# Performance work log

Hardware: AMD Instinct MI355X
Metric: run time of the kernel (lower is better)

The kernel has to match this reference:

```python
import jax, jax.numpy as jnp
import numpy as np

DIM = 1024
HEADS = 16
HEAD_DIM = DIM // HEADS  # 64
B, T, S = 4, 2048, 2048
NEG = -1e9


def rotary_pos_emb(x, freqs):
    # x: (B, H, L, Dh), freqs: (L, Dh//2). Rotate interleaved (even, odd) pairs.
    cos = jnp.cos(freqs)[None, None, :, :]  # (1,1,L,Dh//2)
    sin = jnp.sin(freqs)[None, None, :, :]
    x_even = x[..., 0::2]
    x_odd = x[..., 1::2]
    r_even = x_even * cos - x_odd * sin
    r_odd = x_even * sin + x_odd * cos
    return jnp.stack([r_even, r_odd], axis=-1).reshape(x.shape)


def setup_inputs() -> dict:
    key = jax.random.key(0)
    ks = jax.random.split(key, 9)
    w_std = 1.0 / np.sqrt(DIM)
    return {
        "q_x": jax.random.normal(ks[0], (B, T, DIM), jnp.float32),
        "kv_x": jax.random.normal(ks[1], (B, S, DIM), jnp.float32),
        "freq_q": jax.random.normal(ks[2], (T, HEAD_DIM // 2), jnp.float32),
        "freq_kv": jax.random.normal(ks[3], (S, HEAD_DIM // 2), jnp.float32),
        "key_padding_mask": jax.random.randint(ks[4], (B, S), 0, 2, jnp.int32),
        "Wq": jax.random.normal(ks[5], (DIM, DIM), jnp.float32) * w_std,
        "Wk": jax.random.normal(ks[6], (DIM, DIM), jnp.float32) * w_std,
        "Wv": jax.random.normal(ks[7], (DIM, DIM), jnp.float32) * w_std,
        "Wproj": jax.random.normal(ks[8], (DIM, DIM), jnp.float32) * w_std,
    }


def reference(q_x, kv_x, freq_q, freq_kv, key_padding_mask, Wq, Wk, Wv, Wproj):
    b, t, d = q_x.shape
    s = kv_x.shape[1]
    # QKV projections (torch Linear: x @ W.T), split into heads -> (B, H, L, Dh)
    q = (q_x @ Wq.T).reshape(b, t, HEADS, HEAD_DIM).transpose(0, 2, 1, 3)
    k = (kv_x @ Wk.T).reshape(b, s, HEADS, HEAD_DIM).transpose(0, 2, 1, 3)
    v = (kv_x @ Wv.T).reshape(b, s, HEADS, HEAD_DIM).transpose(0, 2, 1, 3)
    # Rotary embedding on q and k
    q = rotary_pos_emb(q, freq_q)
    k = rotary_pos_emb(k, freq_kv)
    # Scaled dot-product attention with key-padding mask (True = attend)
    scale = HEAD_DIM ** (-0.5)
    scores = jnp.einsum('bhtd,bhsd->bhts', q, k) * scale
    mask = key_padding_mask.astype(bool)[:, None, None, :]  # (B,1,1,S)
    scores = jnp.where(mask, scores, NEG)
    attn = jax.nn.softmax(scores, axis=-1)
    out = jnp.einsum('bhts,bhsd->bhtd', attn, v)
    out = out.transpose(0, 2, 1, 3).reshape(b, t, d)
    return out @ Wproj.T
```

## Files before the change

### kernel.cpp

```cpp
#include <hip/hip_runtime.h>
#include <hip/hip_bf16.h>


typedef __bf16 bf16;
typedef __bf16 bf16x8 __attribute__((ext_vector_type(8)));
typedef __bf16 bf16x4 __attribute__((ext_vector_type(4)));
typedef float  f32x4  __attribute__((ext_vector_type(4)));

#define NB   4
#define NT   2048
#define NS   2048
#define NH   16
#define HD   64
#define SCL  0.18033688011112043f

__device__ __forceinline__ void gload16(const void* g, void* l) {
  __builtin_amdgcn_global_load_lds((const __attribute__((address_space(1))) void*)g,
                                   (__attribute__((address_space(3))) void*)l, 16, 0, 0);
}

__device__ __forceinline__ f32x4 mfma16(bf16x8 a, bf16x8 b, f32x4 c) {
  return __builtin_amdgcn_mfma_f32_16x16x32_bf16(a, b, c, 0, 0, 0);
}

__global__ void k_convert(const float* __restrict__ qx, const float* __restrict__ kvx,
                          const float* __restrict__ Wq, const float* __restrict__ Wk,
                          const float* __restrict__ Wv, const float* __restrict__ Wp,
                          bf16* __restrict__ wbf, bf16* __restrict__ qxbf,
                          bf16* __restrict__ kvxbf)
{
  const long total = 4194304L + 8388608L + 8388608L;
  for (long v = (long)blockIdx.x * blockDim.x + threadIdx.x; v * 4 < total;
       v += (long)gridDim.x * blockDim.x) {
    long e0 = v * 4;
    const float* src; bf16* dst;
    if (e0 < 4194304L) {
      int widx = (int)(e0 >> 20);
      const float* wsrc = (widx == 0) ? Wq : (widx == 1) ? Wk : (widx == 2) ? Wv : Wp;
      src = wsrc + (e0 & 1048575); dst = wbf + e0;
    } else if (e0 < 12582912L) {
      src = qx + (e0 - 4194304L); dst = qxbf + (e0 - 4194304L);
    } else {
      src = kvx + (e0 - 12582912L); dst = kvxbf + (e0 - 12582912L);
    }
    float4 f = *(const float4*)src;
    bf16x4 o = {(bf16)f.x, (bf16)f.y, (bf16)f.z, (bf16)f.w};
    *(bf16x4*)dst = o;
  }
}

__global__ void k_tables(const float* __restrict__ fq, const float* __restrict__ fkv,
                         const int* __restrict__ mask,
                         float2* __restrict__ csq, float2* __restrict__ cskv,
                         float* __restrict__ bias)
{
  int i = blockIdx.x * blockDim.x + threadIdx.x;
  if (i < 65536) {
    float s, c; sincosf(fq[i], &s, &c); csq[i] = make_float2(c, s);
  } else if (i < 131072) {
    int j = i - 65536;
    float s, c; sincosf(fkv[j], &s, &c); cskv[j] = make_float2(c, s);
  } else if (i < 139264) {
    int j = i - 131072;
    bias[j] = mask[j] ? 0.0f : -1.0e9f;
  }
}

template<int EPI>
__global__ __launch_bounds__(256) void k_gemm(
    const bf16* __restrict__ A0, const bf16* __restrict__ A1,
    const bf16* __restrict__ wbase,
    bf16* __restrict__ Qb, bf16* __restrict__ Kb, bf16* __restrict__ Vtb,
    float* __restrict__ Of,
    const float2* __restrict__ csq, const float2* __restrict__ cskv)
{
  __shared__ bf16 As[128 * 32];
  __shared__ bf16 Bs[128 * 32];
  const int z  = (EPI == 0) ? blockIdx.z : 0;
  const bf16* A = (EPI == 1) ? A0 : ((z == 0) ? A0 : A1);
  const bf16* W = wbase + (size_t)z * 1048576;
  const int m0 = blockIdx.x * 128, n0 = blockIdx.y * 128;
  const int tid = threadIdx.x, lane = tid & 63, w = tid >> 6;
  const int g = lane >> 4, c = lane & 15;
  const int wr = w >> 1, wc = w & 1;

  f32x4 acc[4][4];
#pragma unroll
  for (int i = 0; i < 4; ++i)
#pragma unroll
    for (int j = 0; j < 4; ++j) acc[i][j] = 0.0f;

  const bf16* gA = A + (size_t)(m0 + w * 32 + (lane >> 2)) * 1024 + (lane & 3) * 8;
  const bf16* gB = W + (size_t)(n0 + w * 32 + (lane >> 2)) * 1024 + (lane & 3) * 8;
  bf16* lA = As + w * 1024;
  bf16* lB = Bs + w * 1024;

  for (int k0 = 0; k0 < 1024; k0 += 32) {
    __syncthreads();
    gload16(gA, lA);               gload16(gA + 16 * 1024, lA + 512);
    gload16(gB, lB);               gload16(gB + 16 * 1024, lB + 512);
    gA += 32; gB += 32;
    __syncthreads();

    bf16x8 af[4], bfr[4];
#pragma unroll
    for (int mi = 0; mi < 4; ++mi)
      af[mi] = *(const bf16x8*)(As + (wr * 64 + mi * 16 + c) * 32 + g * 8);
#pragma unroll
    for (int ni = 0; ni < 4; ++ni)
      bfr[ni] = *(const bf16x8*)(Bs + (wc * 64 + ni * 16 + c) * 32 + g * 8);
#pragma unroll
    for (int mi = 0; mi < 4; ++mi)
#pragma unroll
      for (int ni = 0; ni < 4; ++ni)
        acc[mi][ni] = mfma16(af[mi], bfr[ni], acc[mi][ni]);
  }

  if (EPI == 1) {
#pragma unroll
    for (int mi = 0; mi < 4; ++mi)
#pragma unroll
      for (int ni = 0; ni < 4; ++ni)
#pragma unroll
        for (int r = 0; r < 4; ++r) {
          int m = m0 + wr * 64 + mi * 16 + g * 4 + r;
          int n = n0 + wc * 64 + ni * 16 + c;
          Of[(size_t)m * 1024 + n] = acc[mi][ni][r];
        }
  } else if (z < 2) {
    const float2* cs = (z == 0) ? csq : cskv;
    bf16* Out = (z == 0) ? Qb : Kb;
#pragma unroll
    for (int mi = 0; mi < 4; ++mi)
#pragma unroll
      for (int ni = 0; ni < 4; ++ni)
#pragma unroll
        for (int r = 0; r < 4; ++r) {
          int m = m0 + wr * 64 + mi * 16 + g * 4 + r;
          int n = n0 + wc * 64 + ni * 16 + c;
          float v = acc[mi][ni][r];
          float p = __shfl_xor(v, 1);
          int t = m & 2047, b = m >> 11;
          int h = n >> 6, d = n & 63;
          float2 cv = cs[t * 32 + (d >> 1)];
          float rot = (d & 1) ? (v * cv.x + p * cv.y)
                              : (v * cv.x - p * cv.y);
          Out[((size_t)((b * 16 + h) * 2048 + t)) * 64 + d] = (bf16)rot;
        }
  } else {
#pragma unroll
    for (int mi = 0; mi < 4; ++mi)
#pragma unroll
      for (int ni = 0; ni < 4; ++ni) {
        int m = m0 + wr * 64 + mi * 16 + g * 4;
        int n = n0 + wc * 64 + ni * 16 + c;
        int b = m >> 11, sl = m & 2047;
        int h = n >> 6, d = n & 63;
        int p  = sl & 63;
        int st = p >> 4, q4 = (p >> 2) & 3;
        int col = (sl & ~63) | ((st >> 1) << 5) | (q4 << 3) | ((st & 1) << 2);
        bf16x4 pk = {(bf16)acc[mi][ni][0], (bf16)acc[mi][ni][1],
                     (bf16)acc[mi][ni][2], (bf16)acc[mi][ni][3]};
        *(bf16x4*)(Vtb + ((size_t)((b * 16 + h) * 64 + d)) * 2048 + col) = pk;
      }
  }
}

__global__ __launch_bounds__(256) void k_attn(
    const bf16* __restrict__ Qb, const bf16* __restrict__ Kb,
    const bf16* __restrict__ Vtb, const float* __restrict__ bias,
    bf16* __restrict__ Ob)
{
  __shared__ bf16 Ks[64 * 64];
  __shared__ bf16 Vs[80 * 64];
  const int bh = blockIdx.y, b = bh >> 4, h = bh & 15;
  const int t0 = blockIdx.x * 64;
  const int tid = threadIdx.x, lane = tid & 63, w = tid >> 6;
  const int g = lane >> 4, c = lane & 15;

  {
    int rr = tid >> 4;
    int col4 = (tid & 15) * 4;
    bf16 v = (rr == 0) ? (bf16)1.0f : (bf16)0.0f;
    bf16x4 vv = {v, v, v, v};
    *(bf16x4*)(Vs + (64 + rr) * 64 + col4) = vv;
  }

  bf16x8 qf[2];
  {
    const bf16* qp = Qb + ((size_t)bh * 2048 + t0 + w * 16 + c) * 64;
    qf[0] = *(const bf16x8*)(qp + g * 8);
    qf[1] = *(const bf16x8*)(qp + 32 + g * 8);
  }

  float mrun = -3.0e38f;
  f32x4 o[5];
#pragma unroll
  for (int ni = 0; ni < 5; ++ni) o[ni] = 0.0f;

  const int srow8 = lane >> 3;
  const int scol  = ((lane & 7) ^ srow8) * 8;
  const bf16* gK = Kb  + ((size_t)bh * 2048 + w * 16 + srow8) * 64 + scol;
  const bf16* gV = Vtb + ((size_t)bh * 64 + w * 16 + srow8) * 2048 + scol;
  bf16* lK = Ks + w * 1024;
  bf16* lV = Vs + w * 1024;
  const float* bp = bias + b * 2048 + g * 4;

  for (int s0 = 0; s0 < 2048; s0 += 64) {
    __syncthreads();
    gload16(gK, lK);            gload16(gK + 512,      lK + 512);
    gload16(gV, lV);            gload16(gV + 8 * 2048, lV + 512);
    gK += 64 * 64; gV += 64;
    float4 bv0 = *(const float4*)(bp + s0);
    float4 bv1 = *(const float4*)(bp + s0 + 16);
    float4 bv2 = *(const float4*)(bp + s0 + 32);
    float4 bv3 = *(const float4*)(bp + s0 + 48);
    __syncthreads();

    f32x4 sc[4];
#pragma unroll
    for (int st = 0; st < 4; ++st) sc[st] = 0.0f;
#pragma unroll
    for (int kd = 0; kd < 2; ++kd)
#pragma unroll
      for (int st = 0; st < 4; ++st) {
        int srow = st * 16 + c;
        bf16x8 kf = *(const bf16x8*)(Ks + srow * 64 + ((kd * 4 + g) ^ (srow & 7)) * 8);
        sc[st] = mfma16(kf, qf[kd], sc[st]);
      }

    float sv[4][4];
#pragma unroll
    for (int r = 0; r < 4; ++r) {
      sv[0][r] = sc[0][r] * SCL + ((const float*)&bv0)[r];
      sv[1][r] = sc[1][r] * SCL + ((const float*)&bv1)[r];
      sv[2][r] = sc[2][r] * SCL + ((const float*)&bv2)[r];
      sv[3][r] = sc[3][r] * SCL + ((const float*)&bv3)[r];
    }

    float mt = sv[0][0];
#pragma unroll
    for (int st = 0; st < 4; ++st)
#pragma unroll
      for (int r = 0; r < 4; ++r) mt = fmaxf(mt, sv[st][r]);
    mt = fmaxf(mt, __shfl_xor(mt, 16));
    mt = fmaxf(mt, __shfl_xor(mt, 32));

    if (__any(mt > mrun + 8.0f)) {
      float mnew = fmaxf(mrun, mt);
      float corr = exp2f(mrun - mnew);
      mrun = mnew;
#pragma unroll
      for (int ni = 0; ni < 5; ++ni) o[ni] *= corr;
    }

    bf16x8 pf[2];
#pragma unroll
    for (int ks = 0; ks < 2; ++ks)
#pragma unroll
      for (int st2 = 0; st2 < 2; ++st2) {
        int st = ks * 2 + st2;
#pragma unroll
        for (int r = 0; r < 4; ++r)
          pf[ks][st2 * 4 + r] = (bf16)exp2f(sv[st][r] - mrun);
      }

#pragma unroll
    for (int ks = 0; ks < 2; ++ks)
#pragma unroll
      for (int ni = 0; ni < 5; ++ni) {
        int vrow = ni * 16 + c;
        bf16x8 vf = *(const bf16x8*)(Vs + vrow * 64 + (((ks * 4 + g) ^ (vrow & 7)) * 8));
        o[ni] = mfma16(vf, pf[ks], o[ni]);
      }
  }

  float l = __shfl(o[4][0], c);
  float rl = 1.0f / l;
  int t = t0 + w * 16 + c;
#pragma unroll
  for (int ni = 0; ni < 4; ++ni) {
    bf16x4 ov = {(bf16)(o[ni][0] * rl), (bf16)(o[ni][1] * rl),
                 (bf16)(o[ni][2] * rl), (bf16)(o[ni][3] * rl)};
    *(bf16x4*)(Ob + ((size_t)(b * 2048 + t)) * 1024 + h * 64 + ni * 16 + g * 4) = ov;
  }
}

extern "C" void kernel_launch(void* const* d_in, const int* in_sizes, int n_in,
                              void* d_out, int out_size, void* d_ws, size_t ws_size,
                              hipStream_t stream)
{
  const float* qx  = (const float*)d_in[0];
  const float* kvx = (const float*)d_in[1];
  const float* fq  = (const float*)d_in[2];
  const float* fkv = (const float*)d_in[3];
  const int*  mask = (const int*)  d_in[4];
  const float* Wq  = (const float*)d_in[5];
  const float* Wk  = (const float*)d_in[6];
  const float* Wv  = (const float*)d_in[7];
  const float* Wp  = (const float*)d_in[8];

  char* ws = (char*)d_ws;
  bf16*   wbf   = (bf16*)(ws);
  bf16*   qxbf  = (bf16*)(ws + 8388608);
  bf16*   kvxbf = (bf16*)(ws + 25165824);
  bf16*   Qb    = (bf16*)(ws + 41943040);
  bf16*   Kb    = (bf16*)(ws + 58720256);
  bf16*   Vtb   = (bf16*)(ws + 75497472);
  bf16*   Ob    = (bf16*)(ws + 92274688);
  float2* csq   = (float2*)(ws + 109051904);
  float2* cskv  = (float2*)(ws + 109576192);
  float*  bias  = (float*)(ws + 110100480);
  float*  out   = (float*)d_out;

  k_convert<<<4096, 256, 0, stream>>>(qx, kvx, Wq, Wk, Wv, Wp, wbf, qxbf, kvxbf);
  k_tables<<<544, 256, 0, stream>>>(fq, fkv, mask, csq, cskv, bias);
  k_gemm<0><<<dim3(64, 8, 3), 256, 0, stream>>>(qxbf, kvxbf, wbf,
                                                Qb, Kb, Vtb, nullptr, csq, cskv);
  k_attn<<<dim3(32, 64), 256, 0, stream>>>(Qb, Kb, Vtb, bias, Ob);
  k_gemm<1><<<dim3(64, 8, 1), 256, 0, stream>>>(Ob, nullptr, wbf + 3 * 1048576,
                                                nullptr, nullptr, nullptr, out, csq, cskv);
}
```

Baseline: 374.6 us.

## Double-buffer K/V tiles, process two query tiles per block, stage bias in LDS

The attention kernel now prefetches the next K/V tile into a second LDS buffer while the current one is computed, replacing the two barriers per iteration with one waitcnt plus barrier. Each block handles 128 query rows (two 64-row tiles) so every K/V fragment read from LDS feeds two MFMAs. The full bias row is loaded into LDS once instead of read from global every iteration, and s_setprio is raised around the MFMA sections. This halves the grid, doubles the accumulator registers, and raises LDS use, which may lower occupancy.

```diff
diff --git a/kernel.cpp b/kernel.cpp
--- a/kernel.cpp
+++ b/kernel.cpp
@@ -171,10 +171,11 @@
     const bf16* __restrict__ Vtb, const float* __restrict__ bias,
     bf16* __restrict__ Ob)
 {
-  __shared__ bf16 Ks[64 * 64];
-  __shared__ bf16 Vs[80 * 64];
+  __shared__ bf16 Ks[2][64 * 64];
+  __shared__ bf16 Vs[2][80 * 64];
+  __shared__ float Bls[2048];
   const int bh = blockIdx.y, b = bh >> 4, h = bh & 15;
-  const int t0 = blockIdx.x * 64;
+  const int t0 = blockIdx.x * 128;
   const int tid = threadIdx.x, lane = tid & 63, w = tid >> 6;
   const int g = lane >> 4, c = lane & 15;
 
@@ -183,106 +184,143 @@
     int col4 = (tid & 15) * 4;
     bf16 v = (rr == 0) ? (bf16)1.0f : (bf16)0.0f;
     bf16x4 vv = {v, v, v, v};
-    *(bf16x4*)(Vs + (64 + rr) * 64 + col4) = vv;
-  }
-
-  bf16x8 qf[2];
+    *(bf16x4*)(&Vs[0][(64 + rr) * 64 + col4]) = vv;
+    *(bf16x4*)(&Vs[1][(64 + rr) * 64 + col4]) = vv;
+  }
   {
-    const bf16* qp = Qb + ((size_t)bh * 2048 + t0 + w * 16 + c) * 64;
-    qf[0] = *(const bf16x8*)(qp + g * 8);
-    qf[1] = *(const bf16x8*)(qp + 32 + g * 8);
-  }
-
-  float mrun = -3.0e38f;
-  f32x4 o[5];
-#pragma unroll
-  for (int ni = 0; ni < 5; ++ni) o[ni] = 0.0f;
+    const float* bsrc = bias + b * 2048;
+    float4 b0 = *(const float4*)(bsrc + tid * 4);
+    float4 b1 = *(const float4*)(bsrc + 1024 + tid * 4);
+    *(float4*)(&Bls[tid * 4]) = b0;
+    *(float4*)(&Bls[1024 + tid * 4]) = b1;
+  }
+
+  bf16x8 qf[2][2];
+#pragma unroll
+  for (int qt = 0; qt < 2; ++qt) {
+    const bf16* qp = Qb + ((size_t)bh * 2048 + t0 + qt * 64 + w * 16 + c) * 64;
+    qf[qt][0] = *(const bf16x8*)(qp + g * 8);
+    qf[qt][1] = *(const bf16x8*)(qp + 32 + g * 8);
+  }
+
+  float mrun[2] = {-3.0e38f, -3.0e38f};
+  f32x4 o[2][5];
+#pragma unroll
+  for (int qt = 0; qt < 2; ++qt)
+#pragma unroll
+    for (int ni = 0; ni < 5; ++ni) o[qt][ni] = 0.0f;
 
   const int srow8 = lane >> 3;
   const int scol  = ((lane & 7) ^ srow8) * 8;
   const bf16* gK = Kb  + ((size_t)bh * 2048 + w * 16 + srow8) * 64 + scol;
   const bf16* gV = Vtb + ((size_t)bh * 64 + w * 16 + srow8) * 2048 + scol;
-  bf16* lK = Ks + w * 1024;
-  bf16* lV = Vs + w * 1024;
-  const float* bp = bias + b * 2048 + g * 4;
-
-  for (int s0 = 0; s0 < 2048; s0 += 64) {
-    __syncthreads();
-    gload16(gK, lK);            gload16(gK + 512,      lK + 512);
-    gload16(gV, lV);            gload16(gV + 8 * 2048, lV + 512);
-    gK += 64 * 64; gV += 64;
-    float4 bv0 = *(const float4*)(bp + s0);
-    float4 bv1 = *(const float4*)(bp + s0 + 16);
-    float4 bv2 = *(const float4*)(bp + s0 + 32);
-    float4 bv3 = *(const float4*)(bp + s0 + 48);
-    __syncthreads();
-
-    f32x4 sc[4];
-#pragma unroll
-    for (int st = 0; st < 4; ++st) sc[st] = 0.0f;
+
+#define STAGE(bufi, ti)  do {                                   \
+    const bf16* k_ = gK + ((size_t)(ti) << 12);                 \
+    const bf16* v_ = gV + (size_t)(ti) * 64;                    \
+    bf16* lk_ = &Ks[bufi][w * 1024];                            \
+    bf16* lv_ = &Vs[bufi][w * 1024];                            \
+    gload16(k_, lk_);            gload16(k_ + 512,      lk_ + 512); \
+    gload16(v_, lv_);            gload16(v_ + 8 * 2048, lv_ + 512); \
+  } while (0)
+
+  STAGE(0, 0);
+  asm volatile("s_waitcnt vmcnt(0)" ::: "memory");
+  __syncthreads();
+
+  for (int ti = 0; ti < 32; ++ti) {
+    const int cur = ti & 1;
+    if (ti < 31) STAGE(cur ^ 1, ti + 1);
+
+    const bf16* KsC = Ks[cur];
+    const bf16* VsC = Vs[cur];
+
+    f32x4 sc[2][4];
+#pragma unroll
+    for (int qt = 0; qt < 2; ++qt)
+#pragma unroll
+      for (int st = 0; st < 4; ++st) sc[qt][st] = 0.0f;
+    __builtin_amdgcn_s_setprio(1);
 #pragma unroll
     for (int kd = 0; kd < 2; ++kd)
 #pragma unroll
       for (int st = 0; st < 4; ++st) {
         int srow = st * 16 + c;
-        bf16x8 kf = *(const bf16x8*)(Ks + srow * 64 + ((kd * 4 + g) ^ (srow & 7)) * 8);
-        sc[st] = mfma16(kf, qf[kd], sc[st]);
+        bf16x8 kf = *(const bf16x8*)(KsC + srow * 64 + ((kd * 4 + g) ^ (srow & 7)) * 8);
+        sc[0][st] = mfma16(kf, qf[0][kd], sc[0][st]);
+        sc[1][st] = mfma16(kf, qf[1][kd], sc[1][st]);
       }
-
-    float sv[4][4];
-#pragma unroll
-    for (int r = 0; r < 4; ++r) {
-      sv[0][r] = sc[0][r] * SCL + ((const float*)&bv0)[r];
-      sv[1][r] = sc[1][r] * SCL + ((const float*)&bv1)[r];
-      sv[2][r] = sc[2][r] * SCL + ((const float*)&bv2)[r];
-      sv[3][r] = sc[3][r] * SCL + ((const float*)&bv3)[r];
+    __builtin_amdgcn_s_setprio(0);
+
+    float4 bv[4];
+#pragma unroll
+    for (int st = 0; st < 4; ++st)
+      bv[st] = *(const float4*)(&Bls[ti * 64 + st * 16 + g * 4]);
+
+    bf16x8 pf[2][2];
+#pragma unroll
+    for (int qt = 0; qt < 2; ++qt) {
+      float sv[4][4];
+#pragma unroll
+      for (int st = 0; st < 4; ++st)
+#pragma unroll
+        for (int r = 0; r < 4; ++r)
+          sv[st][r] = sc[qt][st][r] * SCL + ((const float*)&bv[st])[r];
+
+      float mt = sv[0][0];
+#pragma unroll
+      for (int st = 0; st < 4; ++st)
+#pragma unroll
+        for (int r = 0; r < 4; ++r) mt = fmaxf(mt, sv[st][r]);
+      mt = fmaxf(mt, __shfl_xor(mt, 16));
+      mt = fmaxf(mt, __shfl_xor(mt, 32));
+
+      if (__any(mt > mrun[qt] + 8.0f)) {
+        float mnew = fmaxf(mrun[qt], mt);
+        float corr = exp2f(mrun[qt] - mnew);
+        mrun[qt] = mnew;
+#pragma unroll
+        for (int ni = 0; ni < 5; ++ni) o[qt][ni] *= corr;
+      }
+#pragma unroll
+      for (int ks = 0; ks < 2; ++ks)
+#pragma unroll
+        for (int st2 = 0; st2 < 2; ++st2) {
+          int st = ks * 2 + st2;
+#pragma unroll
+          for (int r = 0; r < 4; ++r)
+            pf[qt][ks][st2 * 4 + r] = (bf16)exp2f(sv[st][r] - mrun[qt]);
+        }
     }
 
-    float mt = sv[0][0];
-#pragma unroll
-    for (int st = 0; st < 4; ++st)
-#pragma unroll
-      for (int r = 0; r < 4; ++r) mt = fmaxf(mt, sv[st][r]);
-    mt = fmaxf(mt, __shfl_xor(mt, 16));
-    mt = fmaxf(mt, __shfl_xor(mt, 32));
-
-    if (__any(mt > mrun + 8.0f)) {
-      float mnew = fmaxf(mrun, mt);
-      float corr = exp2f(mrun - mnew);
-      mrun = mnew;
-#pragma unroll
-      for (int ni = 0; ni < 5; ++ni) o[ni] *= corr;
-    }
-
-    bf16x8 pf[2];
-#pragma unroll
-    for (int ks = 0; ks < 2; ++ks)
-#pragma unroll
-      for (int st2 = 0; st2 < 2; ++st2) {
-        int st = ks * 2 + st2;
-#pragma unroll
-        for (int r = 0; r < 4; ++r)
-          pf[ks][st2 * 4 + r] = (bf16)exp2f(sv[st][r] - mrun);
-      }
-
+    __builtin_amdgcn_s_setprio(1);
 #pragma unroll
     for (int ks = 0; ks < 2; ++ks)
 #pragma unroll
       for (int ni = 0; ni < 5; ++ni) {
         int vrow = ni * 16 + c;
-        bf16x8 vf = *(const bf16x8*)(Vs + vrow * 64 + (((ks * 4 + g) ^ (vrow & 7)) * 8));
-        o[ni] = mfma16(vf, pf[ks], o[ni]);
+        bf16x8 vf = *(const bf16x8*)(VsC + vrow * 64 + (((ks * 4 + g) ^ (vrow & 7)) * 8));
+        o[0][ni] = mfma16(vf, pf[0][ks], o[0][ni]);
+        o[1][ni] = mfma16(vf, pf[1][ks], o[1][ni]);
       }
-  }
-
-  float l = __shfl(o[4][0], c);
-  float rl = 1.0f / l;
-  int t = t0 + w * 16 + c;
-#pragma unroll
-  for (int ni = 0; ni < 4; ++ni) {
-    bf16x4 ov = {(bf16)(o[ni][0] * rl), (bf16)(o[ni][1] * rl),
-                 (bf16)(o[ni][2] * rl), (bf16)(o[ni][3] * rl)};
-    *(bf16x4*)(Ob + ((size_t)(b * 2048 + t)) * 1024 + h * 64 + ni * 16 + g * 4) = ov;
+    __builtin_amdgcn_s_setprio(0);
+
+    asm volatile("s_waitcnt vmcnt(0) lgkmcnt(0)" ::: "memory");
+    __builtin_amdgcn_s_barrier();
+  }
+#undef STAGE
+
+#pragma unroll
+  for (int qt = 0; qt < 2; ++qt) {
+    float l = __shfl(o[qt][4][0], c);
+    float rl = 1.0f / l;
+    int t = t0 + qt * 64 + w * 16 + c;
+#pragma unroll
+    for (int ni = 0; ni < 4; ++ni) {
+      bf16x4 ov = {(bf16)(o[qt][ni][0] * rl), (bf16)(o[qt][ni][1] * rl),
+                   (bf16)(o[qt][ni][2] * rl), (bf16)(o[qt][ni][3] * rl)};
+      *(bf16x4*)(Ob + ((size_t)(b * 2048 + t)) * 1024 + h * 64 + ni * 16 + g * 4) = ov;
+    }
   }
 }
 
@@ -317,7 +355,7 @@
   k_tables<<<544, 256, 0, stream>>>(fq, fkv, mask, csq, cskv, bias);
   k_gemm<0><<<dim3(64, 8, 3), 256, 0, stream>>>(qxbf, kvxbf, wbf,
                                                 Qb, Kb, Vtb, nullptr, csq, cskv);
-  k_attn<<<dim3(32, 64), 256, 0, stream>>>(Qb, Kb, Vtb, bias, Ob);
+  k_attn<<<dim3(16, 64), 256, 0, stream>>>(Qb, Kb, Vtb, bias, Ob);
   k_gemm<1><<<dim3(64, 8, 1), 256, 0, stream>>>(Ob, nullptr, wbf + 3 * 1048576,
                                                 nullptr, nullptr, nullptr, out, csq, cskv);
 }
```

After: 380.5 us. About the same (+1.6%).
